# Kernel optimization log

Hardware: AMD Instinct MI355X
Metric: run time of the kernel (lower is better)

The kernel has to match this reference:

```python
import jax, jax.numpy as jnp
import numpy as np

B, L, D = 512, 64, 16          # batch, lookback, input channels
H, V = 256, 512                # hidden_dim, vector_field_dim
STEPS = 64                     # ode_steps (euler)
EPS = 1e-5


def setup_inputs() -> dict:
    key = jax.random.key(0)
    ks = jax.random.split(key, 8)
    s = lambda fan: 1.0 / np.sqrt(fan)
    return {
        "coeffs": jax.random.normal(ks[0], (B, L - 1, 4, D), jnp.float32) * 0.1,  # cubic spline (a,b,c,d) per interval
        "W0": jax.random.normal(ks[1], (H, D), jnp.float32) * s(D),
        "b0": jnp.zeros((H,), jnp.float32),
        "W1": jax.random.normal(ks[2], (V, H), jnp.float32) * s(H),
        "b1": jnp.zeros((V,), jnp.float32),
        "g1": jnp.ones((V,), jnp.float32),
        "be1": jnp.zeros((V,), jnp.float32),
        "W2": jax.random.normal(ks[3], (V, V), jnp.float32) * s(V),
        "b2": jnp.zeros((V,), jnp.float32),
        "g2": jnp.ones((V,), jnp.float32),
        "be2": jnp.zeros((V,), jnp.float32),
        "W3": jax.random.normal(ks[4], (H * D, V), jnp.float32) * s(V),
        "b3": jnp.zeros((H * D,), jnp.float32),
    }


def _layernorm(x, g, b):
    m = jnp.mean(x, axis=-1, keepdims=True)
    v = jnp.mean((x - m) ** 2, axis=-1, keepdims=True)
    return (x - m) * jax.lax.rsqrt(v + EPS) * g + b


def reference(coeffs, W0, b0, W1, b1, g1, be1, W2, b2, g2, be2, W3, b3):
    # initial projection: h0 = tanh(Linear(X(0))), X(0) = a-coeff of first interval
    X0 = coeffs[:, 0, 0, :]                      # (B, D)
    h0 = jnp.tanh(X0 @ W0.T + b0)                # (B, H)

    t_span = jnp.linspace(0.0, L - 1, STEPS + 1)
    dt = jnp.float32((L - 1) / STEPS)

    def vector_field(h):                         # f(h): (B,H) -> (B,H,D)
        z = jnp.tanh(h @ W1.T + b1)
        z = _layernorm(z, g1, be1)
        z = jnp.tanh(z @ W2.T + b2)
        z = _layernorm(z, g2, be2)
        out = z @ W3.T + b3                      # (B, H*D)
        return out.reshape(h.shape[0], H, D)

    def spline_deriv(t):                         # X'(t): (B, D)
        idx = jnp.clip(jnp.floor(t).astype(jnp.int32), 0, L - 2)
        c = jnp.take(coeffs, idx, axis=1)        # (B, 4, D)
        frac = t - idx.astype(t.dtype)
        return c[:, 1] + 2.0 * frac * c[:, 2] + 3.0 * (frac * frac) * c[:, 3]

    def step(h, t):                              # euler: h += f(h) @ dX
        dX = spline_deriv(t)                     # (B, D)
        h = h + jnp.einsum("bhd,bd->bh", vector_field(h), dX) * dt
        return h, None

    hT, _ = jax.lax.scan(step, h0, t_span[:-1])
    return hT                                    # (B, H) terminal hidden state
```

## Files before the change

kernel.cpp:

```cpp
#include <hip/hip_runtime.h>
#include <hip/hip_bf16.h>

#define B_   512
#define L_   64
#define D_   16
#define H_   256
#define V_   512
#define STEPS_ 64
#define DT_  0.984375f
#define LOSC 2048.0f
#define LOSC_INV (1.0f/2048.0f)

typedef _Float16 half_t;
typedef __attribute__((ext_vector_type(8))) _Float16 half8;
typedef __attribute__((ext_vector_type(4))) float f32x4;

__device__ __forceinline__ void split16(float x, half_t& hi, half_t& lo) {
    half_t h = (half_t)x;
    hi = h;
    lo = (half_t)((x - (float)h) * LOSC);
}


__global__ void pack_frag_kernel(const float* __restrict__ src, half_t* __restrict__ hi,
                                 half_t* __restrict__ lo, int Kc, int K, int total) {
    int idx = blockIdx.x * 256 + threadIdx.x;
    if (idx >= total) return;
    int j = idx & 7;
    int l = (idx >> 3) & 63;
    int gc = idx >> 9;
    int c = gc % Kc, g = gc / Kc;
    int n = (g << 4) + (l & 15);
    int k = (c << 5) + ((l >> 4) << 3) + j;
    float w = src[n * K + k];
    half_t h, lw;
    split16(w, h, lw);
    hi[idx] = h;
    lo[idx] = lw;
}

__global__ void h0_kernel(const float* __restrict__ coeffs, const float* __restrict__ W0,
                          const float* __restrict__ b0, float* __restrict__ hout) {
    int b = blockIdx.x;
    int hh = threadIdx.x;
    float acc = b0[hh];
    #pragma unroll
    for (int d = 0; d < 16; d++)
        acc += coeffs[b * ((L_ - 1) * 4 * D_) + d] * W0[hh * 16 + d];
    hout[b * H_ + hh] = tanhf(acc);
}


__global__ __launch_bounds__(512) void gemm1_kernel(
    const float* __restrict__ hptr,
    const half_t* __restrict__ W1h, const half_t* __restrict__ W1l,
    const float* __restrict__ b1, half_t* __restrict__ t1)
{
    __shared__ __align__(16) half_t Ah[2 * 8 * 64 * 8];
    __shared__ __align__(16) half_t Al[2 * 8 * 64 * 8];
    __shared__ float zs[32][65];
    const int tid = threadIdx.x, w = tid >> 6, l = tid & 63;
    const int row0 = blockIdx.x * 32, col0 = blockIdx.y * 64;

    {
        int gm = w & 1;
        #pragma unroll
        for (int cc = 0; cc < 2; cc++) {
            int c = ((w >> 1) << 1) + cc;
            const float* src = hptr + (row0 + (gm << 4) + (l & 15)) * H_ + (c << 5) + ((l >> 4) << 3);
            float4 x = *(const float4*)src;
            float4 y = *(const float4*)(src + 4);
            float xx[8] = {x.x, x.y, x.z, x.w, y.x, y.y, y.z, y.w};
            half8 hv, lv;
            #pragma unroll
            for (int j = 0; j < 8; j++) { half_t a, b; split16(xx[j], a, b); hv[j] = a; lv[j] = b; }
            int base = (((gm << 3) + c) * 64 + l) * 8;
            *(half8*)&Ah[base] = hv;
            *(half8*)&Al[base] = lv;
        }
    }
    __syncthreads();

    const int mf = w & 1, nf = w >> 1;
    const int gn = (col0 >> 4) + nf;
    f32x4 acc = {0.f, 0.f, 0.f, 0.f}, accl = {0.f, 0.f, 0.f, 0.f};
    for (int c = 0; c < 8; c++) {
        half8 ah = *(const half8*)&Ah[(((mf << 3) + c) * 64 + l) * 8];
        half8 al = *(const half8*)&Al[(((mf << 3) + c) * 64 + l) * 8];
        half8 bh = *(const half8*)&W1h[(((gn << 3) + c) * 64 + l) * 8];
        half8 bl = *(const half8*)&W1l[(((gn << 3) + c) * 64 + l) * 8];
        acc  = __builtin_amdgcn_mfma_f32_16x16x32_f16(ah, bh, acc,  0, 0, 0);
        accl = __builtin_amdgcn_mfma_f32_16x16x32_f16(ah, bl, accl, 0, 0, 0);
        accl = __builtin_amdgcn_mfma_f32_16x16x32_f16(al, bh, accl, 0, 0, 0);
    }
    {
        int colb = (nf << 4) + (l & 15);
        float bb = b1[col0 + colb];
        #pragma unroll
        for (int j = 0; j < 4; j++) {
            float v = acc[j] + accl[j] * LOSC_INV + bb;
            zs[(mf << 4) + ((l >> 4) << 2) + j][colb] = tanhf(v);
        }
    }
    __syncthreads();
    if (tid < 256) {
        int p = tid >> 6;
        int gmp = p & 1, cp = p >> 1;
        half8 hv;
        #pragma unroll
        for (int j = 0; j < 8; j++)
            hv[j] = (half_t)zs[(gmp << 4) + (l & 15)][(cp << 5) + ((l >> 4) << 3) + j];
        *(half8*)&t1[((((row0 >> 4) + gmp) * 16 + (col0 >> 5) + cp) * 64 + l) * 8] = hv;
    }
}

__global__ __launch_bounds__(512) void gemm2_kernel(
    const half_t* __restrict__ t1,
    const float* __restrict__ g1, const float* __restrict__ be1,
    const half_t* __restrict__ W2h, const half_t* __restrict__ W2l,
    const float* __restrict__ b2, half_t* __restrict__ t2)
{
    __shared__ __align__(16) half_t Ah[2 * 16 * 64 * 8];
    __shared__ __align__(16) half_t Al[2 * 16 * 64 * 8];
    __shared__ float part[1024];
    __shared__ float mr[32], rrs[32];
    const int tid = threadIdx.x, w = tid >> 6, l = tid & 63;
    const int row0 = blockIdx.x * 32, col0 = blockIdx.y * 64;
    const int gm = w & 1, cbase = (w >> 1) << 2;

    float tv[32];
    {
        float s = 0.f, ss = 0.f;
        #pragma unroll
        for (int cc = 0; cc < 4; cc++) {
            int c = cbase + cc;
            int base = ((((row0 >> 4) + gm) * 16 + c) * 64 + l) * 8;
            half8 hv = *(const half8*)&t1[base];
            #pragma unroll
            for (int j = 0; j < 8; j++) {
                float t = (float)hv[j];
                tv[(cc << 3) + j] = t;
                s += t; ss += t * t;
            }
        }
        part[w * 64 + l] = s;
        part[512 + w * 64 + l] = ss;
    }
    __syncthreads();
    if (tid < 32) {
        int r = tid, rgm = r >> 4;
        float s = 0.f, ss = 0.f;
        #pragma unroll
        for (int wi = 0; wi < 4; wi++) {
            int wv = rgm + (wi << 1);
            #pragma unroll
            for (int u = 0; u < 4; u++) {
                int idx = wv * 64 + (r & 15) + (u << 4);
                s += part[idx]; ss += part[512 + idx];
            }
        }
        float m = s * (1.f / 512.f);
        float var = ss * (1.f / 512.f) - m * m;
        mr[r] = m;
        rrs[r] = rsqrtf(var + 1e-5f);
    }
    __syncthreads();
    {
        int row = (gm << 4) + (l & 15);
        float m = mr[row], rv = rrs[row];
        #pragma unroll
        for (int cc = 0; cc < 4; cc++) {
            int c = cbase + cc;
            half8 hv, lv;
            #pragma unroll
            for (int j = 0; j < 8; j++) {
                int k = (c << 5) + ((l >> 4) << 3) + j;
                float val = (tv[(cc << 3) + j] - m) * rv * g1[k] + be1[k];
                half_t a, b; split16(val, a, b); hv[j] = a; lv[j] = b;
            }
            int base = (((gm << 4) + c) * 64 + l) * 8;
            *(half8*)&Ah[base] = hv;
            *(half8*)&Al[base] = lv;
        }
    }
    __syncthreads();

    const int mf = w & 1, nf = w >> 1;
    const int gn = (col0 >> 4) + nf;
    f32x4 acc = {0.f, 0.f, 0.f, 0.f}, accl = {0.f, 0.f, 0.f, 0.f};
    for (int c = 0; c < 16; c++) {
        half8 ah = *(const half8*)&Ah[(((mf << 4) + c) * 64 + l) * 8];
        half8 al = *(const half8*)&Al[(((mf << 4) + c) * 64 + l) * 8];
        half8 bh = *(const half8*)&W2h[(((gn << 4) + c) * 64 + l) * 8];
        half8 bl = *(const half8*)&W2l[(((gn << 4) + c) * 64 + l) * 8];
        acc  = __builtin_amdgcn_mfma_f32_16x16x32_f16(ah, bh, acc,  0, 0, 0);
        accl = __builtin_amdgcn_mfma_f32_16x16x32_f16(ah, bl, accl, 0, 0, 0);
        accl = __builtin_amdgcn_mfma_f32_16x16x32_f16(al, bh, accl, 0, 0, 0);
    }
    __syncthreads();
    float (*zs)[65] = (float(*)[65])Ah;
    {
        int colb = (nf << 4) + (l & 15);
        float bb = b2[col0 + colb];
        #pragma unroll
        for (int j = 0; j < 4; j++) {
            float v = acc[j] + accl[j] * LOSC_INV + bb;
            zs[(mf << 4) + ((l >> 4) << 2) + j][colb] = tanhf(v);
        }
    }
    __syncthreads();
    if (tid < 256) {
        int p = tid >> 6;
        int gmp = p & 1, cp = p >> 1;
        half8 hv;
        #pragma unroll
        for (int j = 0; j < 8; j++)
            hv[j] = (half_t)zs[(gmp << 4) + (l & 15)][(cp << 5) + ((l >> 4) << 3) + j];
        *(half8*)&t2[((((row0 >> 4) + gmp) * 16 + (col0 >> 5) + cp) * 64 + l) * 8] = hv;
    }
}

__global__ __launch_bounds__(512) void stage3_kernel(
    const half_t* __restrict__ t2, const half_t* __restrict__ W3h,
    const float* __restrict__ g2, const float* __restrict__ be2,
    const float* __restrict__ b3, const float* __restrict__ coeffs,
    float* __restrict__ hbuf, int ii, float frac)
{
    __shared__ __align__(16) half_t Ah[4 * 16 * 64 * 8];
    __shared__ float dxs[64][17];
    __shared__ float part[256];
    __shared__ float mr[64], rrs[64];
    const int tid = threadIdx.x, w = tid >> 6, l = tid & 63;
    const int rg = blockIdx.x >> 5;
    const int cg = blockIdx.x & 31;
    const int row0 = rg << 6;
    const int gn = (cg << 3) + w;
    const int gm = w >> 1, kh = w & 1;

    for (int idx = tid; idx < 64 * 16; idx += 512) {
        int r = idx >> 4, d = idx & 15;
        int base = ((row0 + r) * (L_ - 1) + ii) * 64 + d;
        float c1 = coeffs[base + 16], c2 = coeffs[base + 32], c3 = coeffs[base + 48];
        dxs[r][d] = c1 + 2.0f * frac * c2 + 3.0f * (frac * frac) * c3;
    }

    {
        float s = 0.f, ss = 0.f;
        #pragma unroll
        for (int cc = 0; cc < 8; cc++) {
            int c = (kh << 3) + cc;
            half8 hv = *(const half8*)&t2[((((rg << 2) + gm) * 16 + c) * 64 + l) * 8];
            *(half8*)&Ah[(((gm << 4) + c) * 64 + l) * 8] = hv;
            #pragma unroll
            for (int j = 0; j < 8; j++) { float t = (float)hv[j]; s += t; ss += t * t; }
        }
        s  += __shfl_xor(s, 16);  s  += __shfl_xor(s, 32);
        ss += __shfl_xor(ss, 16); ss += __shfl_xor(ss, 32);
        if (l < 16) { part[w * 16 + l] = s; part[128 + w * 16 + l] = ss; }
    }
    __syncthreads();
    if (tid < 64) {
        int r = tid;
        int w0 = (r >> 4) << 1, rl = r & 15;
        float s  = part[w0 * 16 + rl] + part[(w0 + 1) * 16 + rl];
        float ss = part[128 + w0 * 16 + rl] + part[128 + (w0 + 1) * 16 + rl];
        float m = s * (1.f / 512.f);
        mr[r] = m;
        rrs[r] = rsqrtf(ss * (1.f / 512.f) - m * m + 1e-5f);
    }
    __syncthreads();
    {
        int r = (gm << 4) + (l & 15);
        float m = mr[r], rv = rrs[r];
        #pragma unroll
        for (int cc = 0; cc < 8; cc++) {
            int c = (kh << 3) + cc;
            int lb = (((gm << 4) + c) * 64 + l) * 8;
            half8 hv = *(const half8*)&Ah[lb];
            int k0 = (c << 5) + ((l >> 4) << 3);
            float4 ga = *(const float4*)&g2[k0];
            float4 gb = *(const float4*)&g2[k0 + 4];
            float4 ba = *(const float4*)&be2[k0];
            float4 bb = *(const float4*)&be2[k0 + 4];
            float gv[8] = {ga.x, ga.y, ga.z, ga.w, gb.x, gb.y, gb.z, gb.w};
            float bv[8] = {ba.x, ba.y, ba.z, ba.w, bb.x, bb.y, bb.z, bb.w};
            half8 ov;
            #pragma unroll
            for (int j = 0; j < 8; j++)
                ov[j] = (half_t)(((float)hv[j] - m) * rv * gv[j] + bv[j]);
            *(half8*)&Ah[lb] = ov;
        }
    }
    __syncthreads();

    f32x4 acc[4];
    #pragma unroll
    for (int i = 0; i < 4; i++) acc[i] = (f32x4){0, 0, 0, 0};
    for (int c = 0; c < 16; c++) {
        half8 bh = *(const half8*)&W3h[(((gn << 4) + c) * 64 + l) * 8];
        #pragma unroll
        for (int mf = 0; mf < 4; mf++) {
            half8 ah = *(const half8*)&Ah[(((mf << 4) + c) * 64 + l) * 8];
            acc[mf] = __builtin_amdgcn_mfma_f32_16x16x32_f16(ah, bh, acc[mf], 0, 0, 0);
        }
    }

    const int d = l & 15;
    const float b3v = b3[(gn << 4) + d];
    #pragma unroll
    for (int mf = 0; mf < 4; mf++) {
        #pragma unroll
        for (int j = 0; j < 4; j++) {
            int rl = (mf << 4) + ((l >> 4) << 2) + j;
            float s = (acc[mf][j] + b3v) * dxs[rl][d];
            s += __shfl_xor(s, 1);
            s += __shfl_xor(s, 2);
            s += __shfl_xor(s, 4);
            s += __shfl_xor(s, 8);
            if (d == 0) hbuf[(row0 + rl) * H_ + gn] += s * DT_;
        }
    }
}


extern "C" void kernel_launch(void* const* d_in, const int* in_sizes, int n_in,
                              void* d_out, int out_size, void* d_ws, size_t ws_size,
                              hipStream_t stream) {
    const float* coeffs = (const float*)d_in[0];
    const float* W0  = (const float*)d_in[1];
    const float* b0  = (const float*)d_in[2];
    const float* W1  = (const float*)d_in[3];
    const float* b1  = (const float*)d_in[4];
    const float* g1  = (const float*)d_in[5];
    const float* be1 = (const float*)d_in[6];
    const float* W2  = (const float*)d_in[7];
    const float* b2  = (const float*)d_in[8];
    const float* g2  = (const float*)d_in[9];
    const float* be2 = (const float*)d_in[10];
    const float* W3  = (const float*)d_in[11];
    const float* b3  = (const float*)d_in[12];

    char* w = (char*)d_ws;
    float*  hbuf = (float*)(w);
    half_t* t1   = (half_t*)(w + 524288);
    half_t* t2   = (half_t*)(w + 1048576);
    half_t* W1h  = (half_t*)(w + 1572864);
    half_t* W1l  = (half_t*)(w + 1835008);
    half_t* W2h  = (half_t*)(w + 2097152);
    half_t* W2l  = (half_t*)(w + 2621440);
    half_t* W3h  = (half_t*)(w + 3145728);
    half_t* W3l  = (half_t*)(w + 7340032);

    pack_frag_kernel<<<512, 256, 0, stream>>>(W1, W1h, W1l, 8, H_, V_ * H_);
    pack_frag_kernel<<<1024, 256, 0, stream>>>(W2, W2h, W2l, 16, V_, V_ * V_);
    pack_frag_kernel<<<8192, 256, 0, stream>>>(W3, W3h, W3l, 16, V_, (H_ * D_) * V_);
    h0_kernel<<<B_, H_, 0, stream>>>(coeffs, W0, b0, hbuf);

    for (int s = 0; s < STEPS_; s++) {
        float t = (float)s * 0.984375f;
        int ii = (int)t;
        if (ii > L_ - 2) ii = L_ - 2;
        float frac = t - (float)ii;
        gemm1_kernel<<<dim3(16, 8), 512, 0, stream>>>(hbuf, W1h, W1l, b1, t1);
        gemm2_kernel<<<dim3(16, 8), 512, 0, stream>>>(t1, g1, be1, W2h, W2l, b2, t2);
        stage3_kernel<<<256, 512, 0, stream>>>(t2, W3h, g2, be2, b3, coeffs,
                                               hbuf, ii, frac);
    }

    hipMemcpyAsync(d_out, hbuf, (size_t)B_ * H_ * sizeof(float),
                   hipMemcpyDeviceToDevice, stream);
}
```

Measured before the change: 1.698 ms.

## Fold LayerNorm affine into weights and emit row stats from producer GEMM epilogues

LayerNorm gamma is folded into W2 and W3 at pack time. Beta and bias are folded into per-column vectors, so each LN becomes a per-row rescale r*S - m*r*cg + cb applied in the next GEMM's epilogue. The producing kernels now write partial row sums and sums of squares to global stats buffers, so gemm2 and stage3 can feed t1/t2 straight into MFMA without an LDS normalize pass. This drops one of the three split-precision MFMAs in gemm2 (A is no longer split), at the cost of extra rounding and cancellation in the affine reformulation applied to fp16 activations.

```diff
diff --git a/kernel.cpp b/kernel.cpp
--- a/kernel.cpp
+++ b/kernel.cpp
@@ -39,6 +39,57 @@
     lo[idx] = lw;
 }
 
+__global__ void pack_frag_scaled2_kernel(const float* __restrict__ src,
+                                         const float* __restrict__ scale,
+                                         half_t* __restrict__ hi, half_t* __restrict__ lo,
+                                         int Kc, int K, int total) {
+    int idx = blockIdx.x * 256 + threadIdx.x;
+    if (idx >= total) return;
+    int j = idx & 7;
+    int l = (idx >> 3) & 63;
+    int gc = idx >> 9;
+    int c = gc % Kc, g = gc / Kc;
+    int n = (g << 4) + (l & 15);
+    int k = (c << 5) + ((l >> 4) << 3) + j;
+    float w = src[n * K + k] * scale[k];
+    half_t h, lw;
+    split16(w, h, lw);
+    hi[idx] = h;
+    lo[idx] = lw;
+}
+
+__global__ void pack_frag_scaled1_kernel(const float* __restrict__ src,
+                                         const float* __restrict__ scale,
+                                         half_t* __restrict__ hi,
+                                         int Kc, int K, int total) {
+    int idx = blockIdx.x * 256 + threadIdx.x;
+    if (idx >= total) return;
+    int j = idx & 7;
+    int l = (idx >> 3) & 63;
+    int gc = idx >> 9;
+    int c = gc % Kc, g = gc / Kc;
+    int n = (g << 4) + (l & 15);
+    int k = (c << 5) + ((l >> 4) << 3) + j;
+    hi[idx] = (half_t)(src[n * K + k] * scale[k]);
+}
+
+__global__ void colvec_kernel(const float* __restrict__ W, const float* __restrict__ g,
+                              const float* __restrict__ be, const float* __restrict__ b,
+                              float* __restrict__ cg, float* __restrict__ cb, int N, int K) {
+    int n = blockIdx.x * 4 + (threadIdx.x >> 6);
+    if (n >= N) return;
+    int l = threadIdx.x & 63;
+    float sg = 0.f, sb = 0.f;
+    for (int k = l; k < K; k += 64) {
+        float w = W[n * K + k];
+        sg += g[k] * w;
+        sb += be[k] * w;
+    }
+    #pragma unroll
+    for (int o = 32; o; o >>= 1) { sg += __shfl_xor(sg, o); sb += __shfl_xor(sb, o); }
+    if (l == 0) { cg[n] = sg; cb[n] = sb + b[n]; }
+}
+
 __global__ void h0_kernel(const float* __restrict__ coeffs, const float* __restrict__ W0,
                           const float* __restrict__ b0, float* __restrict__ hout) {
     int b = blockIdx.x;
@@ -54,7 +105,8 @@
 __global__ __launch_bounds__(512) void gemm1_kernel(
     const float* __restrict__ hptr,
     const half_t* __restrict__ W1h, const half_t* __restrict__ W1l,
-    const float* __restrict__ b1, half_t* __restrict__ t1)
+    const float* __restrict__ b1, half_t* __restrict__ t1,
+    float* __restrict__ stats1, int sIdx)
 {
     __shared__ __align__(16) half_t Ah[2 * 8 * 64 * 8];
     __shared__ __align__(16) half_t Al[2 * 8 * 64 * 8];
@@ -103,6 +155,18 @@
         }
     }
     __syncthreads();
+    {
+        int r = tid >> 4, c0 = (tid & 15) << 2;
+        float s = 0.f, ss = 0.f;
+        #pragma unroll
+        for (int j = 0; j < 4; j++) { float v = zs[r][c0 + j]; s += v; ss += v * v; }
+        #pragma unroll
+        for (int o = 8; o; o >>= 1) { s += __shfl_xor(s, o); ss += __shfl_xor(ss, o); }
+        if ((tid & 15) == 0) {
+            float* st = stats1 + (((sIdx << 3) + blockIdx.y) * 512 + row0 + r) * 2;
+            st[0] = s; st[1] = ss;
+        }
+    }
     if (tid < 256) {
         int p = tid >> 6;
         int gmp = p & 1, cp = p >> 1;
@@ -115,100 +179,65 @@
 }
 
 __global__ __launch_bounds__(512) void gemm2_kernel(
-    const half_t* __restrict__ t1,
-    const float* __restrict__ g1, const float* __restrict__ be1,
-    const half_t* __restrict__ W2h, const half_t* __restrict__ W2l,
-    const float* __restrict__ b2, half_t* __restrict__ t2)
+    const half_t* __restrict__ t1, const float* __restrict__ stats1,
+    const half_t* __restrict__ W2gh, const half_t* __restrict__ W2gl,
+    const float* __restrict__ cg2, const float* __restrict__ cb2,
+    half_t* __restrict__ t2, float* __restrict__ stats2, int sIdx)
 {
-    __shared__ __align__(16) half_t Ah[2 * 16 * 64 * 8];
-    __shared__ __align__(16) half_t Al[2 * 16 * 64 * 8];
-    __shared__ float part[1024];
+    __shared__ float zs[32][65];
     __shared__ float mr[32], rrs[32];
     const int tid = threadIdx.x, w = tid >> 6, l = tid & 63;
     const int row0 = blockIdx.x * 32, col0 = blockIdx.y * 64;
-    const int gm = w & 1, cbase = (w >> 1) << 2;
-
-    float tv[32];
-    {
+
+    if (tid < 32) {
         float s = 0.f, ss = 0.f;
         #pragma unroll
-        for (int cc = 0; cc < 4; cc++) {
-            int c = cbase + cc;
-            int base = ((((row0 >> 4) + gm) * 16 + c) * 64 + l) * 8;
-            half8 hv = *(const half8*)&t1[base];
-            #pragma unroll
-            for (int j = 0; j < 8; j++) {
-                float t = (float)hv[j];
-                tv[(cc << 3) + j] = t;
-                s += t; ss += t * t;
-            }
-        }
-        part[w * 64 + l] = s;
-        part[512 + w * 64 + l] = ss;
-    }
-    __syncthreads();
-    if (tid < 32) {
-        int r = tid, rgm = r >> 4;
-        float s = 0.f, ss = 0.f;
-        #pragma unroll
-        for (int wi = 0; wi < 4; wi++) {
-            int wv = rgm + (wi << 1);
-            #pragma unroll
-            for (int u = 0; u < 4; u++) {
-                int idx = wv * 64 + (r & 15) + (u << 4);
-                s += part[idx]; ss += part[512 + idx];
-            }
+        for (int p = 0; p < 8; p++) {
+            const float* st = stats1 + (((sIdx << 3) + p) * 512 + row0 + tid) * 2;
+            s += st[0]; ss += st[1];
         }
         float m = s * (1.f / 512.f);
-        float var = ss * (1.f / 512.f) - m * m;
-        mr[r] = m;
-        rrs[r] = rsqrtf(var + 1e-5f);
-    }
-    __syncthreads();
-    {
-        int row = (gm << 4) + (l & 15);
-        float m = mr[row], rv = rrs[row];
-        #pragma unroll
-        for (int cc = 0; cc < 4; cc++) {
-            int c = cbase + cc;
-            half8 hv, lv;
-            #pragma unroll
-            for (int j = 0; j < 8; j++) {
-                int k = (c << 5) + ((l >> 4) << 3) + j;
-                float val = (tv[(cc << 3) + j] - m) * rv * g1[k] + be1[k];
-                half_t a, b; split16(val, a, b); hv[j] = a; lv[j] = b;
-            }
-            int base = (((gm << 4) + c) * 64 + l) * 8;
-            *(half8*)&Ah[base] = hv;
-            *(half8*)&Al[base] = lv;
-        }
+        mr[tid] = m;
+        rrs[tid] = rsqrtf(ss * (1.f / 512.f) - m * m + 1e-5f);
     }
     __syncthreads();
 
     const int mf = w & 1, nf = w >> 1;
     const int gn = (col0 >> 4) + nf;
+    const int gmA = (row0 >> 4) + mf;
     f32x4 acc = {0.f, 0.f, 0.f, 0.f}, accl = {0.f, 0.f, 0.f, 0.f};
     for (int c = 0; c < 16; c++) {
-        half8 ah = *(const half8*)&Ah[(((mf << 4) + c) * 64 + l) * 8];
-        half8 al = *(const half8*)&Al[(((mf << 4) + c) * 64 + l) * 8];
-        half8 bh = *(const half8*)&W2h[(((gn << 4) + c) * 64 + l) * 8];
-        half8 bl = *(const half8*)&W2l[(((gn << 4) + c) * 64 + l) * 8];
+        half8 ah = *(const half8*)&t1[((gmA * 16 + c) * 64 + l) * 8];
+        half8 bh = *(const half8*)&W2gh[(((gn << 4) + c) * 64 + l) * 8];
+        half8 bl = *(const half8*)&W2gl[(((gn << 4) + c) * 64 + l) * 8];
         acc  = __builtin_amdgcn_mfma_f32_16x16x32_f16(ah, bh, acc,  0, 0, 0);
         accl = __builtin_amdgcn_mfma_f32_16x16x32_f16(ah, bl, accl, 0, 0, 0);
-        accl = __builtin_amdgcn_mfma_f32_16x16x32_f16(al, bh, accl, 0, 0, 0);
-    }
-    __syncthreads();
-    float (*zs)[65] = (float(*)[65])Ah;
+    }
     {
         int colb = (nf << 4) + (l & 15);
-        float bb = b2[col0 + colb];
+        int col = col0 + colb;
+        float cgv = cg2[col], cbv = cb2[col];
         #pragma unroll
         for (int j = 0; j < 4; j++) {
-            float v = acc[j] + accl[j] * LOSC_INV + bb;
-            zs[(mf << 4) + ((l >> 4) << 2) + j][colb] = tanhf(v);
-        }
-    }
-    __syncthreads();
+            int r = (mf << 4) + ((l >> 4) << 2) + j;
+            float S = acc[j] + accl[j] * LOSC_INV;
+            float v = rrs[r] * S - mr[r] * rrs[r] * cgv + cbv;
+            zs[r][colb] = tanhf(v);
+        }
+    }
+    __syncthreads();
+    {
+        int r = tid >> 4, c0 = (tid & 15) << 2;
+        float s = 0.f, ss = 0.f;
+        #pragma unroll
+        for (int j = 0; j < 4; j++) { float v = zs[r][c0 + j]; s += v; ss += v * v; }
+        #pragma unroll
+        for (int o = 8; o; o >>= 1) { s += __shfl_xor(s, o); ss += __shfl_xor(ss, o); }
+        if ((tid & 15) == 0) {
+            float* st = stats2 + (((sIdx << 3) + blockIdx.y) * 512 + row0 + r) * 2;
+            st[0] = s; st[1] = ss;
+        }
+    }
     if (tid < 256) {
         int p = tid >> 6;
         int gmp = p & 1, cp = p >> 1;
@@ -221,20 +250,19 @@
 }
 
 __global__ __launch_bounds__(512) void stage3_kernel(
-    const half_t* __restrict__ t2, const half_t* __restrict__ W3h,
-    const float* __restrict__ g2, const float* __restrict__ be2,
-    const float* __restrict__ b3, const float* __restrict__ coeffs,
-    float* __restrict__ hbuf, int ii, float frac)
+    const half_t* __restrict__ t2, const float* __restrict__ stats2,
+    const half_t* __restrict__ W3gh, const float* __restrict__ cg3,
+    const float* __restrict__ cb3, const float* __restrict__ coeffs,
+    float* __restrict__ hbuf, int ii, float frac, int sIdx)
 {
     __shared__ __align__(16) half_t Ah[4 * 16 * 64 * 8];
     __shared__ float dxs[64][17];
-    __shared__ float part[256];
-    __shared__ float mr[64], rrs[64];
+    __shared__ float mvals[64], rvals[64];
     const int tid = threadIdx.x, w = tid >> 6, l = tid & 63;
     const int rg = blockIdx.x >> 5;
-    const int cg = blockIdx.x & 31;
+    const int cgi = blockIdx.x & 31;
     const int row0 = rg << 6;
-    const int gn = (cg << 3) + w;
+    const int gn = (cgi << 3) + w;
     const int gm = w >> 1, kh = w & 1;
 
     for (int idx = tid; idx < 64 * 16; idx += 512) {
@@ -243,53 +271,22 @@
         float c1 = coeffs[base + 16], c2 = coeffs[base + 32], c3 = coeffs[base + 48];
         dxs[r][d] = c1 + 2.0f * frac * c2 + 3.0f * (frac * frac) * c3;
     }
-
-    {
+    if (tid < 64) {
         float s = 0.f, ss = 0.f;
         #pragma unroll
-        for (int cc = 0; cc < 8; cc++) {
-            int c = (kh << 3) + cc;
-            half8 hv = *(const half8*)&t2[((((rg << 2) + gm) * 16 + c) * 64 + l) * 8];
-            *(half8*)&Ah[(((gm << 4) + c) * 64 + l) * 8] = hv;
-            #pragma unroll
-            for (int j = 0; j < 8; j++) { float t = (float)hv[j]; s += t; ss += t * t; }
-        }
-        s  += __shfl_xor(s, 16);  s  += __shfl_xor(s, 32);
-        ss += __shfl_xor(ss, 16); ss += __shfl_xor(ss, 32);
-        if (l < 16) { part[w * 16 + l] = s; part[128 + w * 16 + l] = ss; }
-    }
-    __syncthreads();
-    if (tid < 64) {
-        int r = tid;
-        int w0 = (r >> 4) << 1, rl = r & 15;
-        float s  = part[w0 * 16 + rl] + part[(w0 + 1) * 16 + rl];
-        float ss = part[128 + w0 * 16 + rl] + part[128 + (w0 + 1) * 16 + rl];
+        for (int p = 0; p < 8; p++) {
+            const float* st = stats2 + (((sIdx << 3) + p) * 512 + row0 + tid) * 2;
+            s += st[0]; ss += st[1];
+        }
         float m = s * (1.f / 512.f);
-        mr[r] = m;
-        rrs[r] = rsqrtf(ss * (1.f / 512.f) - m * m + 1e-5f);
-    }
-    __syncthreads();
-    {
-        int r = (gm << 4) + (l & 15);
-        float m = mr[r], rv = rrs[r];
-        #pragma unroll
-        for (int cc = 0; cc < 8; cc++) {
-            int c = (kh << 3) + cc;
-            int lb = (((gm << 4) + c) * 64 + l) * 8;
-            half8 hv = *(const half8*)&Ah[lb];
-            int k0 = (c << 5) + ((l >> 4) << 3);
-            float4 ga = *(const float4*)&g2[k0];
-            float4 gb = *(const float4*)&g2[k0 + 4];
-            float4 ba = *(const float4*)&be2[k0];
-            float4 bb = *(const float4*)&be2[k0 + 4];
-            float gv[8] = {ga.x, ga.y, ga.z, ga.w, gb.x, gb.y, gb.z, gb.w};
-            float bv[8] = {ba.x, ba.y, ba.z, ba.w, bb.x, bb.y, bb.z, bb.w};
-            half8 ov;
-            #pragma unroll
-            for (int j = 0; j < 8; j++)
-                ov[j] = (half_t)(((float)hv[j] - m) * rv * gv[j] + bv[j]);
-            *(half8*)&Ah[lb] = ov;
-        }
+        mvals[tid] = m;
+        rvals[tid] = rsqrtf(ss * (1.f / 512.f) - m * m + 1e-5f);
+    }
+    #pragma unroll
+    for (int cc = 0; cc < 8; cc++) {
+        int c = (kh << 3) + cc;
+        half8 hv = *(const half8*)&t2[((((rg << 2) + gm) * 16 + c) * 64 + l) * 8];
+        *(half8*)&Ah[(((gm << 4) + c) * 64 + l) * 8] = hv;
     }
     __syncthreads();
 
@@ -297,7 +294,7 @@
     #pragma unroll
     for (int i = 0; i < 4; i++) acc[i] = (f32x4){0, 0, 0, 0};
     for (int c = 0; c < 16; c++) {
-        half8 bh = *(const half8*)&W3h[(((gn << 4) + c) * 64 + l) * 8];
+        half8 bh = *(const half8*)&W3gh[(((gn << 4) + c) * 64 + l) * 8];
         #pragma unroll
         for (int mf = 0; mf < 4; mf++) {
             half8 ah = *(const half8*)&Ah[(((mf << 4) + c) * 64 + l) * 8];
@@ -306,13 +303,15 @@
     }
 
     const int d = l & 15;
-    const float b3v = b3[(gn << 4) + d];
+    const int o = (gn << 4) + d;
+    const float cgv = cg3[o], cbv = cb3[o];
     #pragma unroll
     for (int mf = 0; mf < 4; mf++) {
         #pragma unroll
         for (int j = 0; j < 4; j++) {
             int rl = (mf << 4) + ((l >> 4) << 2) + j;
-            float s = (acc[mf][j] + b3v) * dxs[rl][d];
+            float vf = rvals[rl] * acc[mf][j] - mvals[rl] * rvals[rl] * cgv + cbv;
+            float s = vf * dxs[rl][d];
             s += __shfl_xor(s, 1);
             s += __shfl_xor(s, 2);
             s += __shfl_xor(s, 4);
@@ -341,19 +340,26 @@
     const float* b3  = (const float*)d_in[12];
 
     char* w = (char*)d_ws;
-    float*  hbuf = (float*)(w);
-    half_t* t1   = (half_t*)(w + 524288);
-    half_t* t2   = (half_t*)(w + 1048576);
-    half_t* W1h  = (half_t*)(w + 1572864);
-    half_t* W1l  = (half_t*)(w + 1835008);
-    half_t* W2h  = (half_t*)(w + 2097152);
-    half_t* W2l  = (half_t*)(w + 2621440);
-    half_t* W3h  = (half_t*)(w + 3145728);
-    half_t* W3l  = (half_t*)(w + 7340032);
+    float*  hbuf   = (float*)(w);
+    half_t* t1     = (half_t*)(w + 524288);
+    half_t* t2     = (half_t*)(w + 1048576);
+    half_t* W1h    = (half_t*)(w + 1572864);
+    half_t* W1l    = (half_t*)(w + 1835008);
+    half_t* W2gh   = (half_t*)(w + 2097152);
+    half_t* W2gl   = (half_t*)(w + 2621440);
+    half_t* W3gh   = (half_t*)(w + 3145728);
+    float*  cg2    = (float*)(w + 7340032);
+    float*  cb2    = (float*)(w + 7342080);
+    float*  cg3    = (float*)(w + 7344128);
+    float*  cb3    = (float*)(w + 7360512);
+    float*  stats1 = (float*)(w + 7376896);
+    float*  stats2 = (float*)(w + 9474048);
 
     pack_frag_kernel<<<512, 256, 0, stream>>>(W1, W1h, W1l, 8, H_, V_ * H_);
-    pack_frag_kernel<<<1024, 256, 0, stream>>>(W2, W2h, W2l, 16, V_, V_ * V_);
-    pack_frag_kernel<<<8192, 256, 0, stream>>>(W3, W3h, W3l, 16, V_, (H_ * D_) * V_);
+    pack_frag_scaled2_kernel<<<1024, 256, 0, stream>>>(W2, g1, W2gh, W2gl, 16, V_, V_ * V_);
+    pack_frag_scaled1_kernel<<<8192, 256, 0, stream>>>(W3, g2, W3gh, 16, V_, (H_ * D_) * V_);
+    colvec_kernel<<<V_ / 4, 256, 0, stream>>>(W2, g1, be1, b2, cg2, cb2, V_, V_);
+    colvec_kernel<<<(H_ * D_) / 4, 256, 0, stream>>>(W3, g2, be2, b3, cg3, cb3, H_ * D_, V_);
     h0_kernel<<<B_, H_, 0, stream>>>(coeffs, W0, b0, hbuf);
 
     for (int s = 0; s < STEPS_; s++) {
@@ -361,10 +367,11 @@
         int ii = (int)t;
         if (ii > L_ - 2) ii = L_ - 2;
         float frac = t - (float)ii;
-        gemm1_kernel<<<dim3(16, 8), 512, 0, stream>>>(hbuf, W1h, W1l, b1, t1);
-        gemm2_kernel<<<dim3(16, 8), 512, 0, stream>>>(t1, g1, be1, W2h, W2l, b2, t2);
-        stage3_kernel<<<256, 512, 0, stream>>>(t2, W3h, g2, be2, b3, coeffs,
-                                               hbuf, ii, frac);
+        gemm1_kernel<<<dim3(16, 8), 512, 0, stream>>>(hbuf, W1h, W1l, b1, t1, stats1, s);
+        gemm2_kernel<<<dim3(16, 8), 512, 0, stream>>>(t1, stats1, W2gh, W2gl,
+                                                      cg2, cb2, t2, stats2, s);
+        stage3_kernel<<<256, 512, 0, stream>>>(t2, stats2, W3gh, cg3, cb3, coeffs,
+                                               hbuf, ii, frac, s);
     }
 
     hipMemcpyAsync(d_out, hbuf, (size_t)B_ * H_ * sizeof(float),
```

Measured after the change: 1.520 ms. 1.12x faster.
